# Optimization experiments

Measured on AMD Instinct MI355X. Metric: run time of the kernel, lower is better.

Reference implementation:

```python
import jax, jax.numpy as jnp
import numpy as np

B, NWORD, HID = 4, 24, 512


def setup_inputs() -> dict:
    key = jax.random.key(0)
    ks = jax.random.split(key, 7)
    H = HID
    scale_in = 1.0 / np.sqrt(H)
    return {
        "seqt": jax.random.normal(ks[0], (B, NWORD, 2 * H), dtype=jnp.float32),
        # ins_input_linearity: Linear(H -> 5H) with bias
        "Wi": jax.random.normal(ks[1], (5 * H, H), dtype=jnp.float32) * scale_in,
        "bi": jnp.zeros((5 * H,), dtype=jnp.float32),
        # ins_state_linearity: Linear(H -> 5H) with bias (bias init: forget slots = 1)
        "Ws": jax.random.normal(ks[2], (5 * H, H), dtype=jnp.float32) * scale_in,
        "bs": jnp.zeros((5 * H,), dtype=jnp.float32).at[H:2 * H].set(1.0),
        # ins_bilinearity: BilinearSimilarity(2H, 2H) -> scalar x^T W y
        "Wbil": jax.random.normal(ks[3], (2 * H, 2 * H), dtype=jnp.float32) * (1.0 / (2.0 * H)),
    }


def reference(seqt, Wi, bi, Ws, bs, Wbil):
    """Inside pass (do_inside) of DioLstm in training mode (soft_sum over splits).

    Chart cell (left, L) covers words [left, left+L]. Returns root v = concat(h, c).
    """
    Bn, n, twoH = seqt.shape
    H = twoH // 2
    # ins_bias buffer: ones on the two forget-gate slots [H:3H]
    ins_bias = jnp.zeros((5 * H,), dtype=seqt.dtype).at[H:3 * H].set(1.0)

    def single(seq):  # seq: [n, 2H]
        chartH = jnp.zeros((n, n, H), seq.dtype).at[:, 0].set(seq[:, :H])
        chartC = jnp.zeros((n, n, H), seq.dtype).at[:, 0].set(seq[:, H:])
        chartS = jnp.zeros((n, n), seq.dtype)  # leaf scores are 0
        for L in range(1, n):  # span length - 1 (static unroll over diagonals)
            P = n - L  # number of spans on this diagonal
            lefts = jnp.arange(P)[:, None]          # [P,1]
            ksplit = jnp.arange(L)[None, :]          # [1,L]
            # left child: (left, k); right child: (left+k+1, L-1-k)
            lH = chartH[lefts, ksplit]; lC = chartC[lefts, ksplit]; lS = chartS[lefts, ksplit]
            ridx = lefts + ksplit + 1
            rlen = jnp.broadcast_to(L - 1 - ksplit, ridx.shape)
            rH = chartH[ridx, rlen]; rC = chartC[ridx, rlen]; rS = chartS[ridx, rlen]
            lv = jnp.concatenate([lH, lC], axis=-1)  # [P,L,2H]
            rv = jnp.concatenate([rH, rC], axis=-1)
            # bilinear compatibility + child scores
            compat = jnp.einsum('pki,ij,pkj->pk', lv, Wbil, rv) + lS + rS  # [P,L]
            # projected_input + projected_state (sum once; gate slices of the sum)
            proj = (lH @ Wi.T + bi + ins_bias) + (rH @ Ws.T + bs)  # [P,L,5H]
            ig, lf, rf, g, og = jnp.split(proj, 5, axis=-1)
            ig = jax.nn.sigmoid(ig); lf = jax.nn.sigmoid(lf); rf = jax.nn.sigmoid(rf)
            g = jnp.tanh(g); og = jax.nn.sigmoid(og)
            mem = lf * lC + rf * rC + ig * g
            h = og * jnp.tanh(mem)  # [P,L,H]
            # soft_sum: torch.tensor(s_set) detaches scores -> stop_gradient on weights
            sw = jax.lax.stop_gradient(compat)
            w = jax.nn.softmax(sw, axis=-1)  # [P,L]
            Hnew = jnp.einsum('pk,pkh->ph', w, h)
            Cnew = jnp.einsum('pk,pkh->ph', w, mem)
            Snew = jnp.sum(w * sw, axis=-1)
            pidx = jnp.arange(P)
            chartH = chartH.at[pidx, L].set(Hnew)
            chartC = chartC.at[pidx, L].set(Cnew)
            chartS = chartS.at[pidx, L].set(Snew)
        # root cell v = concat(h, c)
        return jnp.concatenate([chartH[0, n - 1], chartC[0, n - 1]], axis=0)

    return jax.vmap(single)(seqt)  # [B, 2H]
```

## Files before the change

kernel.cpp:

```cpp
#include <hip/hip_runtime.h>
#include <math.h>

#define NB 4
#define NW 24
#define H 512
#define H2 1024
#define H5 2560
#define NCELL 300
#define NEED_BYTES ((size_t)72<<20)

static float* g_buf = nullptr;
__attribute__((constructor)) static void dio_alloc_ws(){
  (void)hipMalloc((void**)&g_buf, NEED_BYTES);
}

typedef __attribute__((ext_vector_type(8))) short bf16x8;
typedef __attribute__((ext_vector_type(4))) float f32x4;
typedef unsigned short ushort_t;

__device__ __forceinline__ int coff(int l){ return l*NW - (l*(l-1))/2; }
__device__ __forceinline__ float sigm(float x){ return 1.f/(1.f+__expf(-x)); }
__device__ __forceinline__ float ftanh(float x){ return 1.f - 2.f/(__expf(2.f*x)+1.f); }

__device__ __forceinline__ ushort_t f2b(float x){
  unsigned int u = __float_as_uint(x);
  u += 0x7FFF + ((u>>16)&1);
  return (ushort_t)(u>>16);
}
__device__ __forceinline__ float b2f(ushort_t h){
  return __uint_as_float(((unsigned int)h)<<16);
}
__device__ __forceinline__ void split_store(ushort_t* __restrict__ ph,
                                            ushort_t* __restrict__ pl,
                                            size_t idx, float x){
  ushort_t h = f2b(x);
  ph[idx] = h;
  pl[idx] = f2b(x - b2f(h));
}

__device__ __forceinline__ void gload_lds16(const void* g, void* l){
  __builtin_amdgcn_global_load_lds(
      (const __attribute__((address_space(1))) unsigned int*)g,
      (__attribute__((address_space(3))) unsigned int*)l, 16, 0, 0);
}

__device__ __forceinline__ float compat_dot(const float* __restrict__ cU,
                                            const float* __restrict__ cH,
                                            const float* __restrict__ cC,
                                            const float* __restrict__ cS,
                                            int lc, int rc, int lane){
  const float4* U4  = (const float4*)(cU + (size_t)lc*H2);
  const float4* Hr4 = (const float4*)(cH + (size_t)rc*H);
  const float4* Cr4 = (const float4*)(cC + (size_t)rc*H);
  float p = 0.f;
  #pragma unroll
  for (int it=0; it<2; it++){
    float4 u = U4[lane + 64*it], h = Hr4[lane + 64*it];
    p += u.x*h.x + u.y*h.y + u.z*h.z + u.w*h.w;
  }
  #pragma unroll
  for (int it=0; it<2; it++){
    float4 u = U4[128 + lane + 64*it], c = Cr4[lane + 64*it];
    p += u.x*c.x + u.y*c.y + u.z*c.z + u.w*c.w;
  }
  #pragma unroll
  for (int off=32; off>0; off>>=1) p += __shfl_down(p, off);
  return p + cS[lc] + cS[rc];
}

__global__ void k_init(const float* __restrict__ seqt,
                       const float* __restrict__ Wi, const float* __restrict__ Ws,
                       const float* __restrict__ Wbil,
                       ushort_t* __restrict__ WWblob, ushort_t* __restrict__ WBblob,
                       float* __restrict__ cH, float* __restrict__ cC, float* __restrict__ cS,
                       ushort_t* __restrict__ cHbh, ushort_t* __restrict__ cHbl,
                       ushort_t* __restrict__ cCbh, ushort_t* __restrict__ cCbl){
  const int blk = blockIdx.x, t = threadIdx.x;
  if (blk < 1280){
    const int gid = blk*256 + t;
    const int half = 163840;
    const float* mat = (gid < half) ? Wi : Ws;
    const int cid = (gid < half) ? gid : gid - half;
    const int j = cid >> 6;
    const int c0 = (cid & 63) << 3;
    const int tile = ((gid < half) ? 0 : 160) + (j >> 4);
    const int row = j & 15;
    const float4* s = (const float4*)(mat + (size_t)j*H + c0);
    float4 a = s[0], b4 = s[1];
    float xs[8] = {a.x,a.y,a.z,a.w, b4.x,b4.y,b4.z,b4.w};
    union { ushort_t u[8]; bf16x8 v; } hh, ll;
    #pragma unroll
    for (int i=0;i<8;i++){
      ushort_t h = f2b(xs[i]);
      hh.u[i] = h; ll.u[i] = f2b(xs[i] - b2f(h));
    }
    char* base = (char*)WWblob + (size_t)tile*32768;
    const int off = ((row<<10) + (c0<<1)) ^ ((row&7)<<4);
    *(bf16x8*)(base + off) = hh.v;
    *(bf16x8*)(base + 16384 + off) = ll.v;
  } else if (blk < 2304){
    __shared__ float tile[32][33];
    int tb = blk - 1280;
    int tr = (tb>>5)*32, tc = (tb&31)*32;
    int tx = t & 31, ty = t >> 5;
    #pragma unroll
    for (int i=0;i<32;i+=8)
      tile[ty+i][tx] = Wbil[(size_t)(tr+ty+i)*H2 + tc+tx];
    __syncthreads();
    if (t < 128){
      const int c = t & 31, r0 = (t >> 5) << 3;
      const int jg = tc + c;
      const int k0 = tr + r0;
      union { ushort_t u[8]; bf16x8 v; } hh, ll;
      #pragma unroll
      for (int i=0;i<8;i++){
        float x = tile[r0+i][c];
        ushort_t h = f2b(x);
        hh.u[i] = h; ll.u[i] = f2b(x - b2f(h));
      }
      char* base = (char*)WBblob + (size_t)(jg>>4)*65536;
      const int row = jg & 15;
      const int off = ((row<<11) + (k0<<1)) ^ ((row&7)<<4);
      *(bf16x8*)(base + off) = hh.v;
      *(bf16x8*)(base + 32768 + off) = ll.v;
    }
  } else {
    int tid = (blk-2304)*256 + t;
    if (tid < NB*NW*H){
      int b = tid/(NW*H); int r = tid%(NW*H); int i = r/H; int d = r%H;
      size_t idx = (size_t)(b*NCELL + i)*H + d;
      float hv = seqt[(size_t)(b*NW+i)*H2 + d];
      float cv = seqt[(size_t)(b*NW+i)*H2 + H + d];
      cH[idx]=hv; cC[idx]=cv;
      split_store(cHbh,cHbl,idx,hv);
      split_store(cCbh,cCbl,idx,cv);
      if (d==0) cS[b*NCELL+i] = 0.f;
    }
  }
}

__device__ __forceinline__ void mfma3(f32x4& acc, bf16x8 ah, bf16x8 al,
                                      bf16x8 bh, bf16x8 bl){
  acc = __builtin_amdgcn_mfma_f32_16x16x32_bf16(ah, bh, acc, 0,0,0);
  acc = __builtin_amdgcn_mfma_f32_16x16x32_bf16(ah, bl, acc, 0,0,0);
  acc = __builtin_amdgcn_mfma_f32_16x16x32_bf16(al, bh, acc, 0,0,0);
}

__global__ void __launch_bounds__(512)
k_proj3(const ushort_t* __restrict__ WWblob, const ushort_t* __restrict__ WBblob,
        const float* __restrict__ bi, const float* __restrict__ bs,
        const ushort_t* __restrict__ cHbh, const ushort_t* __restrict__ cHbl,
        const ushort_t* __restrict__ cCbh, const ushort_t* __restrict__ cCbl,
        float* __restrict__ cPI, float* __restrict__ cPS, float* __restrict__ cU,
        int d, int P)
{
  __shared__ __attribute__((aligned(16))) ushort_t wlds[32768];
  __shared__ f32x4 red[8][64];
  const int t = threadIdx.x, wv = t>>6, lane = t&63;
  const int r = lane & 15;
  const int q = lane >> 4;
  const int jt = blockIdx.x;

  int kind, j0;
  if (jt < 160){ kind=0; j0 = jt*16; }
  else if (jt < 320){ kind=1; j0 = (jt-160)*16; }
  else { kind=2; j0 = (jt-320)*16; }

  {
    const char* blob = (kind < 2)
        ? (const char*)WWblob + (size_t)jt*32768
        : (const char*)WBblob + (size_t)(jt-320)*65536;
    const int nseg = (kind < 2) ? 4 : 8;
    for (int i = 0; i < nseg; i++){
      const int lo = i*8192 + wv*1024;
      gload_lds16(blob + lo + lane*16, (char*)wlds + lo);
    }
    asm volatile("s_waitcnt vmcnt(0)" ::: "memory");
  }
  __syncthreads();

  const int Mtot = NB*P, mt = (Mtot+15)>>4;
  const int swz = (r&7)<<4;
  const char* wb = (const char*)wlds;
  const int jo = j0 + r;
  float bias = 0.f;
  if (kind==0) bias = bi[jo] + ((jo>=H && jo<3*H)?1.f:0.f);
  else if (kind==1) bias = bs[jo];

  const f32x4 z4 = {0.f,0.f,0.f,0.f};
  const int units = 2*mt;
  const int rounds = (units + 7) >> 3;
  for (int rd = 0; rd < rounds; rd++){
    const int u = rd*8 + wv;
    const int half = u & 1;
    const int mtile = u >> 1;
    f32x4 sA = z4;
    int m0 = 0, nm = 0;
    if (u < units){
      m0 = mtile*16;
      nm = min(16, Mtot - m0);
      const int mg = m0 + (r < nm ? r : 0);
      const size_t arow = (size_t)((mg/P)*NCELL + coff(d) + mg%P)*H;
      f32x4 acc[4];
      #pragma unroll
      for (int wi=0;wi<4;wi++) acc[wi] = z4;
      if (kind < 2){
        #pragma unroll
        for (int wi=0; wi<4; wi++){
          const int w = half*4 + wi;
          #pragma unroll
          for (int s=0;s<2;s++){
            const int ko = w*64 + q*8 + s*32;
            bf16x8 ah = *(const bf16x8*)(cHbh + arow + ko);
            bf16x8 al = *(const bf16x8*)(cHbl + arow + ko);
            const int bo = ((r<<10) + (ko<<1)) ^ swz;
            bf16x8 bh = *(const bf16x8*)(wb + bo);
            bf16x8 bl = *(const bf16x8*)(wb + 16384 + bo);
            mfma3(acc[wi], ah, al, bh, bl);
          }
        }
      } else {
        const ushort_t* ah_ = (half==0 ? cHbh : cCbh) + arow;
        const ushort_t* al_ = (half==0 ? cHbl : cCbl) + arow;
        #pragma unroll
        for (int wi=0; wi<4; wi++){
          const int w = half*4 + wi;
          const int kg0 = w*128, ka0 = kg0 & 511;
          #pragma unroll
          for (int s=0;s<4;s++){
            const int so = s*32 + q*8;
            bf16x8 ah = *(const bf16x8*)(ah_ + ka0 + so);
            bf16x8 al = *(const bf16x8*)(al_ + ka0 + so);
            const int bo = ((r<<11) + ((kg0+so)<<1)) ^ swz;
            bf16x8 bh = *(const bf16x8*)(wb + bo);
            bf16x8 bl = *(const bf16x8*)(wb + 32768 + bo);
            mfma3(acc[wi], ah, al, bh, bl);
          }
        }
      }
      sA = (acc[0]+acc[1]) + (acc[2]+acc[3]);
    }
    red[wv][lane] = sA;
    __syncthreads();
    if (half==0 && u < units){
      f32x4 tot = red[wv][lane] + red[wv|1][lane];
      #pragma unroll
      for (int reg=0; reg<4; reg++){
        const int m = q*4 + reg;
        if (m < nm){
          const int mg2 = m0 + m;
          const size_t cell = (size_t)((mg2/P)*NCELL + coff(d) + mg2%P);
          const float v = tot[reg];
          if (kind==0)      cPI[cell*H5 + jo] = v + bias;
          else if (kind==1) cPS[cell*H5 + jo] = v + bias;
          else              cU [cell*H2 + jo] = v;
        }
      }
    }
    __syncthreads();
  }
}

__global__ void __launch_bounds__(256)
k_combine3(const float* __restrict__ cPI, const float* __restrict__ cPS,
           const float* __restrict__ cU,
           float* __restrict__ cH, float* __restrict__ cC, float* __restrict__ cS,
           ushort_t* __restrict__ cHbh, ushort_t* __restrict__ cHbl,
           ushort_t* __restrict__ cCbh, ushort_t* __restrict__ cCbl,
           const float* __restrict__ compatR, float* __restrict__ compatW,
           float* __restrict__ out, int L, int P){
  const int t = threadIdx.x;
  const int lane = t & 63;
  const int wave = t >> 6;
  const int nphase = NB*P*16;
  const int blk = blockIdx.x;

  if (blk >= nphase){
    const int P1 = P-1;
    const int nterm = L-1;
    int tid = (blk-nphase)*4 + wave;
    if (P1 > 0 && nterm > 0 && tid < NB*P1*nterm){
      int cell1 = tid / nterm;
      int k = 1 + tid % nterm;
      int b = cell1 / P1, left = cell1 % P1;
      int lc = b*NCELL + coff(k) + left;
      int rc = b*NCELL + coff(L-k) + left+k+1;
      float v = compat_dot(cU, cH, cC, cS, lc, rc, lane);
      if (lane==0) compatW[(b*NW + left)*NW + k] = v;
    }
    return;
  }

  const int cellid = blk >> 4;
  const int dg = blk & 15;
  const int b = cellid / P;
  const int left = cellid % P;
  __shared__ float compat_s[32];
  __shared__ float wts_s[32];
  __shared__ float S_s;
  __shared__ float partH[8][32];
  __shared__ float partC[8][32];

  if (wave == 0){
    int lc = b*NCELL + left;
    int rc = b*NCELL + coff(L-1) + left+1;
    float v = compat_dot(cU, cH, cC, cS, lc, rc, lane);
    if (lane==0) compat_s[0] = v;
  } else if (wave == 1 && L >= 2){
    int lc = b*NCELL + coff(L-1) + left;
    int rc = b*NCELL + left+L;
    float v = compat_dot(cU, cH, cC, cS, lc, rc, lane);
    if (lane==0) compat_s[L-1] = v;
  }
  if (t >= 1 && t <= L-2) compat_s[t] = compatR[(b*NW + left)*NW + t];
  __syncthreads();
  if (t==0){
    float mx = -1e30f;
    for (int k=0;k<L;k++) mx = fmaxf(mx, compat_s[k]);
    float den = 0.f;
    for (int k=0;k<L;k++){ float e = __expf(compat_s[k]-mx); wts_s[k]=e; den+=e; }
    float inv = 1.f/den, S = 0.f;
    for (int k=0;k<L;k++){ wts_s[k]*=inv; S += wts_s[k]*compat_s[k]; }
    S_s = S;
  }
  __syncthreads();
  const int dloc = t & 31;
  const int dim = dg*32 + dloc;
  const int kpar = t >> 5;
  float aH = 0.f, aC = 0.f;
  for (int k=kpar; k<L; k+=8){
    float wk = wts_s[k];
    int lc = b*NCELL + coff(k) + left;
    int rc = b*NCELL + coff(L-1-k) + left+k+1;
    const float* PI = cPI + (size_t)lc*H5;
    const float* PS = cPS + (size_t)rc*H5;
    float p0 = PI[dim]     + PS[dim];
    float p1 = PI[H+dim]   + PS[H+dim];
    float p2 = PI[2*H+dim] + PS[2*H+dim];
    float p3 = PI[3*H+dim] + PS[3*H+dim];
    float p4 = PI[4*H+dim] + PS[4*H+dim];
    float lcv = cC[(size_t)lc*H + dim];
    float rcv = cC[(size_t)rc*H + dim];
    float mem = sigm(p1)*lcv + sigm(p2)*rcv + sigm(p0)*ftanh(p3);
    float h = sigm(p4)*ftanh(mem);
    aH += wk*h; aC += wk*mem;
  }
  if (kpar > 0){ partH[kpar][dloc]=aH; partC[kpar][dloc]=aC; }
  __syncthreads();
  if (kpar == 0){
    #pragma unroll
    for (int q=1;q<8;q++){ aH += partH[q][dloc]; aC += partC[q][dloc]; }
    if (L == NW-1){
      out[b*H2 + dim]     = aH;
      out[b*H2 + H + dim] = aC;
      return;
    }
    size_t nc = (size_t)(b*NCELL + coff(L) + left);
    cH[nc*H + dim] = aH;
    cC[nc*H + dim] = aC;
    split_store(cHbh,cHbl, nc*H + dim, aH);
    split_store(cCbh,cCbl, nc*H + dim, aC);
    if (t==0 && dg==0) cS[nc] = S_s;
  }
}

extern "C" void kernel_launch(void* const* d_in, const int* in_sizes, int n_in,
                              void* d_out, int out_size, void* d_ws, size_t ws_size,
                              hipStream_t stream){
  const float* seqt = (const float*)d_in[0];
  const float* Wi   = (const float*)d_in[1];
  const float* bi   = (const float*)d_in[2];
  const float* Ws   = (const float*)d_in[3];
  const float* bs   = (const float*)d_in[4];
  const float* Wbil = (const float*)d_in[5];
  float* out = (float*)d_out;

  float* p = (ws_size >= NEED_BYTES && g_buf == nullptr) ? (float*)d_ws : g_buf;
  float* cH  = p; p += (size_t)NB*NCELL*H;
  float* cC  = p; p += (size_t)NB*NCELL*H;
  float* cS  = p; p += (size_t)NB*NCELL;
  float* cPI = p; p += (size_t)NB*NCELL*H5;
  float* cPS = p; p += (size_t)NB*NCELL*H5;
  float* cU  = p; p += (size_t)NB*NCELL*H2;
  float* compatA = p; p += (size_t)NB*NW*NW;
  float* compatB = p; p += (size_t)NB*NW*NW;
  ushort_t* u = (ushort_t*)p;
  ushort_t* WWblob = u; u += (size_t)320*16384;
  ushort_t* WBblob = u; u += (size_t)64*32768;
  ushort_t* cHbh   = u; u += (size_t)NB*NCELL*H;
  ushort_t* cHbl   = u; u += (size_t)NB*NCELL*H;
  ushort_t* cCbh   = u; u += (size_t)NB*NCELL*H;
  ushort_t* cCbl   = u; u += (size_t)NB*NCELL*H;

  k_init<<<2496, 256, 0, stream>>>(seqt, Wi, Ws, Wbil,
      WWblob, WBblob, cH, cC, cS, cHbh, cHbl, cCbh, cCbl);

  k_proj3<<<384, 512, 0, stream>>>(
      WWblob, WBblob, bi, bs,
      cHbh, cHbl, cCbh, cCbl, cPI, cPS, cU, 0, NW);
  for (int L=1; L<NW; L++){
    int P = NW - L;
    int P1 = P-1, nterm = L-1;
    int wblk = (P1>0 && nterm>0) ? (NB*P1*nterm + 3)/4 : 0;
    float* bufR = (L&1) ? compatA : compatB;
    float* bufW = (L&1) ? compatB : compatA;
    k_combine3<<<NB*P*16 + wblk, 256, 0, stream>>>(
        cPI, cPS, cU, cH, cC, cS, cHbh, cHbl, cCbh, cCbl,
        bufR, bufW, out, L, P);
    if (L < NW-1)
      k_proj3<<<384, 512, 0, stream>>>(
          WWblob, WBblob, bi, bs,
          cHbh, cHbl, cCbh, cCbl, cPI, cPS, cU, L, P);
  }
}
```

Baseline: 577.9 us.

## Precompute interior-split LSTM gates in extra projection blocks ahead of combine

Adds extra blocks to the projection kernel that evaluate the LSTM gate math (h and mem) for every interior split of the next diagonal whose children are already final, writing them to new gH/gM buffers. The combine kernel then loads precomputed h/mem for interior splits and recomputes only the two edge splits that depend on the freshly projected cells. This moves most gate work off the serial combine critical path and overlaps it with the GEMM blocks. The cost is extra global buffers and writes/reads of h and mem per split.

```diff
diff --git a/kernel.cpp b/kernel.cpp
--- a/kernel.cpp
+++ b/kernel.cpp
@@ -147,19 +147,50 @@
 }
 
 __global__ void __launch_bounds__(512)
-k_proj3(const ushort_t* __restrict__ WWblob, const ushort_t* __restrict__ WBblob,
+k_proj4(const ushort_t* __restrict__ WWblob, const ushort_t* __restrict__ WBblob,
         const float* __restrict__ bi, const float* __restrict__ bs,
         const ushort_t* __restrict__ cHbh, const ushort_t* __restrict__ cHbl,
         const ushort_t* __restrict__ cCbh, const ushort_t* __restrict__ cCbl,
+        const float* __restrict__ cC,
         float* __restrict__ cPI, float* __restrict__ cPS, float* __restrict__ cU,
+        float* __restrict__ gH, float* __restrict__ gM,
         int d, int P)
 {
   __shared__ __attribute__((aligned(16))) ushort_t wlds[32768];
   __shared__ f32x4 red[8][64];
   const int t = threadIdx.x, wv = t>>6, lane = t&63;
+  const int jt = blockIdx.x;
+
+  if (jt >= 384){
+    const int Ln = d + 1;
+    const int nk = Ln - 2;
+    const int Pg = NW - Ln;
+    const int gi = jt - 384;
+    const int b = gi / (Pg*nk), rr = gi % (Pg*nk);
+    const int left = rr / nk;
+    const int k = 1 + rr % nk;
+    const int lc = b*NCELL + coff(k) + left;
+    const int rc = b*NCELL + coff(Ln-1-k) + left+k+1;
+    const float* PI = cPI + (size_t)lc*H5;
+    const float* PS = cPS + (size_t)rc*H5;
+    const int dim = t;
+    float p0 = PI[dim]     + PS[dim];
+    float p1 = PI[H+dim]   + PS[H+dim];
+    float p2 = PI[2*H+dim] + PS[2*H+dim];
+    float p3 = PI[3*H+dim] + PS[3*H+dim];
+    float p4 = PI[4*H+dim] + PS[4*H+dim];
+    float lcv = cC[(size_t)lc*H + dim];
+    float rcv = cC[(size_t)rc*H + dim];
+    float mem = sigm(p1)*lcv + sigm(p2)*rcv + sigm(p0)*ftanh(p3);
+    float h = sigm(p4)*ftanh(mem);
+    const size_t gidx = ((size_t)(b*NW + left)*NW + k)*H + dim;
+    gH[gidx] = h;
+    gM[gidx] = mem;
+    return;
+  }
+
   const int r = lane & 15;
   const int q = lane >> 4;
-  const int jt = blockIdx.x;
 
   int kind, j0;
   if (jt < 160){ kind=0; j0 = jt*16; }
@@ -262,12 +293,13 @@
 }
 
 __global__ void __launch_bounds__(256)
-k_combine3(const float* __restrict__ cPI, const float* __restrict__ cPS,
+k_combine4(const float* __restrict__ cPI, const float* __restrict__ cPS,
            const float* __restrict__ cU,
            float* __restrict__ cH, float* __restrict__ cC, float* __restrict__ cS,
            ushort_t* __restrict__ cHbh, ushort_t* __restrict__ cHbl,
            ushort_t* __restrict__ cCbh, ushort_t* __restrict__ cCbl,
            const float* __restrict__ compatR, float* __restrict__ compatW,
+           const float* __restrict__ gH, const float* __restrict__ gM,
            float* __restrict__ out, int L, int P){
   const int t = threadIdx.x;
   const int lane = t & 63;
@@ -330,19 +362,26 @@
   float aH = 0.f, aC = 0.f;
   for (int k=kpar; k<L; k+=8){
     float wk = wts_s[k];
-    int lc = b*NCELL + coff(k) + left;
-    int rc = b*NCELL + coff(L-1-k) + left+k+1;
-    const float* PI = cPI + (size_t)lc*H5;
-    const float* PS = cPS + (size_t)rc*H5;
-    float p0 = PI[dim]     + PS[dim];
-    float p1 = PI[H+dim]   + PS[H+dim];
-    float p2 = PI[2*H+dim] + PS[2*H+dim];
-    float p3 = PI[3*H+dim] + PS[3*H+dim];
-    float p4 = PI[4*H+dim] + PS[4*H+dim];
-    float lcv = cC[(size_t)lc*H + dim];
-    float rcv = cC[(size_t)rc*H + dim];
-    float mem = sigm(p1)*lcv + sigm(p2)*rcv + sigm(p0)*ftanh(p3);
-    float h = sigm(p4)*ftanh(mem);
+    float mem, h;
+    if (k == 0 || k == L-1){
+      int lc = b*NCELL + coff(k) + left;
+      int rc = b*NCELL + coff(L-1-k) + left+k+1;
+      const float* PI = cPI + (size_t)lc*H5;
+      const float* PS = cPS + (size_t)rc*H5;
+      float p0 = PI[dim]     + PS[dim];
+      float p1 = PI[H+dim]   + PS[H+dim];
+      float p2 = PI[2*H+dim] + PS[2*H+dim];
+      float p3 = PI[3*H+dim] + PS[3*H+dim];
+      float p4 = PI[4*H+dim] + PS[4*H+dim];
+      float lcv = cC[(size_t)lc*H + dim];
+      float rcv = cC[(size_t)rc*H + dim];
+      mem = sigm(p1)*lcv + sigm(p2)*rcv + sigm(p0)*ftanh(p3);
+      h = sigm(p4)*ftanh(mem);
+    } else {
+      const size_t gidx = ((size_t)(b*NW + left)*NW + k)*H + dim;
+      h = gH[gidx];
+      mem = gM[gidx];
+    }
     aH += wk*h; aC += wk*mem;
   }
   if (kpar > 0){ partH[kpar][dloc]=aH; partC[kpar][dloc]=aC; }
@@ -384,6 +423,8 @@
   float* cU  = p; p += (size_t)NB*NCELL*H2;
   float* compatA = p; p += (size_t)NB*NW*NW;
   float* compatB = p; p += (size_t)NB*NW*NW;
+  float* gH  = p; p += (size_t)NB*NW*NW*H;
+  float* gM  = p; p += (size_t)NB*NW*NW*H;
   ushort_t* u = (ushort_t*)p;
   ushort_t* WWblob = u; u += (size_t)320*16384;
   ushort_t* WBblob = u; u += (size_t)64*32768;
@@ -395,21 +436,24 @@
   k_init<<<2496, 256, 0, stream>>>(seqt, Wi, Ws, Wbil,
       WWblob, WBblob, cH, cC, cS, cHbh, cHbl, cCbh, cCbl);
 
-  k_proj3<<<384, 512, 0, stream>>>(
+  k_proj4<<<384, 512, 0, stream>>>(
       WWblob, WBblob, bi, bs,
-      cHbh, cHbl, cCbh, cCbl, cPI, cPS, cU, 0, NW);
+      cHbh, cHbl, cCbh, cCbl, cC, cPI, cPS, cU, gH, gM, 0, NW);
   for (int L=1; L<NW; L++){
     int P = NW - L;
     int P1 = P-1, nterm = L-1;
     int wblk = (P1>0 && nterm>0) ? (NB*P1*nterm + 3)/4 : 0;
     float* bufR = (L&1) ? compatA : compatB;
     float* bufW = (L&1) ? compatB : compatA;
-    k_combine3<<<NB*P*16 + wblk, 256, 0, stream>>>(
+    k_combine4<<<NB*P*16 + wblk, 256, 0, stream>>>(
         cPI, cPS, cU, cH, cC, cS, cHbh, cHbl, cCbh, cCbl,
-        bufR, bufW, out, L, P);
-    if (L < NW-1)
-      k_proj3<<<384, 512, 0, stream>>>(
+        bufR, bufW, gH, gM, out, L, P);
+    if (L < NW-1){
+      int Ln = L + 1;
+      int ngate = (Ln >= 3) ? NB*(NW-Ln)*(Ln-2) : 0;
+      k_proj4<<<384 + ngate, 512, 0, stream>>>(
           WWblob, WBblob, bi, bs,
-          cHbh, cHbl, cCbh, cCbl, cPI, cPS, cU, L, P);
-  }
-}
+          cHbh, cHbl, cCbh, cCbl, cC, cPI, cPS, cU, gH, gM, L, P);
+    }
+  }
+}
```

New measurement: 566.9 us, median of 2. Within noise of the previous version (-1.9%).
